# Optimization experiments

Hardware: AMD Instinct MI355X
Metric: run time of the kernel (lower is better)

The kernel has to match this reference:

```python
import jax, jax.numpy as jnp
import numpy as np

B, H, V, L, T = 64, 512, 32000, 3, 38
SOS = 0  # word2idx['<SOS>']


def setup_inputs() -> dict:
    key = jax.random.key(0)
    ks = jax.random.split(key, 16)
    s = 0.05
    rn = lambda k, shape: jax.random.normal(k, shape, jnp.float32) * s
    return {
        "feat": jax.random.normal(ks[0], (B, H), jnp.float32),
        "W_ih0": rn(ks[1], (4 * H, 2 * H)),
        "W_hh0": rn(ks[2], (4 * H, H)),
        "W_ih_rest": rn(ks[3], (L - 1, 4 * H, H)),
        "W_hh_rest": rn(ks[4], (L - 1, 4 * H, H)),
        "b_ih": rn(ks[5], (L, 4 * H)),
        "b_hh": rn(ks[6], (L, 4 * H)),
        "embed": rn(ks[7], (V, H)),
        "W_proj": rn(ks[8], (V, H)),
        "b_proj": rn(ks[9], (V,)),
        "W_hid": rn(ks[10], (H, H)),
        "b_hid": rn(ks[11], (H,)),
        "W_enc": rn(ks[12], (H, H)),
        "b_enc": rn(ks[13], (H,)),
        "W_attout": rn(ks[14], (1, H)),
        "b_attout": rn(ks[15], (1,)),
    }


def _lstm_cell(x, h, c, Wih, Whh, bih, bhh):
    # PyTorch gate order: i, f, g, o
    g = x @ Wih.T + h @ Whh.T + bih + bhh
    i, f, gg, o = jnp.split(g, 4, axis=-1)
    c2 = jax.nn.sigmoid(f) * c + jax.nn.sigmoid(i) * jnp.tanh(gg)
    h2 = jax.nn.sigmoid(o) * jnp.tanh(c2)
    return h2, c2


def _forward(feat, W_ih0, W_hh0, W_ih_rest, W_hh_rest, b_ih, b_hh,
             embed, W_proj, b_proj, W_hid, b_hid, W_enc, b_enc,
             W_attout, b_attout):
    # encoder 'sequence': pooled feature repeated over L decoder layers -> [L,B,H]
    enc = jnp.broadcast_to(feat[None], (L, B, H))
    enc_p = enc @ W_enc.T + b_enc  # precompute encoder projection (constant over steps)

    def attn(hbar):  # hbar = sum(hidden_layers)/L, [B,H]  (Bahdanau additive attention)
        e = (jnp.tanh(enc_p + (hbar @ W_hid.T + b_hid)[None]) @ W_attout.T + b_attout)[..., 0]  # [L,B]
        w = jax.nn.softmax(e, axis=0)  # softmax over encoder positions
        return jnp.einsum('lb,lbh->bh', w, enc)  # context [B,H]

    def lstm(inp, h, c):  # one time-step through the 3-layer stacked LSTM
        h0, c0 = _lstm_cell(inp, h[0], c[0], W_ih0, W_hh0, b_ih[0], b_hh[0])
        h1, c1 = _lstm_cell(h0, h[1], c[1], W_ih_rest[0], W_hh_rest[0], b_ih[1], b_hh[1])
        h2, c2 = _lstm_cell(h1, h[2], c[2], W_ih_rest[1], W_hh_rest[1], b_ih[2], b_hh[2])
        return jnp.stack([h0, h1, h2]), jnp.stack([c0, c1, c2])

    ctx0 = attn(feat)  # initial hidden = feat repeated L times -> mean = feat
    start = jnp.broadcast_to(embed[SOS], (B, H))
    h = jnp.broadcast_to(ctx0[None], (L, B, H))
    c = h
    inp0 = jnp.concatenate([ctx0, start], axis=-1)  # [B, 2H]

    def step(carry, _):
        h, c, inp = carry
        h, c = lstm(inp, h, c)
        out = h[-1]  # [B,H]
        ids = jnp.argmax(out @ W_proj.T + b_proj, axis=-1)  # greedy token (dropout in eval mode)
        emb = embed[ids]  # [B,H]
        ctx = attn(emb / L)  # addMask averages with 1/decoder_layer weights
        return (h, c, jnp.concatenate([ctx, emb], axis=-1)), out

    _, outs = jax.lax.scan(step, (h, c, inp0), None, length=T - 1)  # outs [T-1,B,H]
    pred = jnp.concatenate([start[None], outs], axis=0)  # [T,B,H]
    # final projection, permuted to [B, V, T] as in the torch module
    return jnp.einsum('tbh,vh->bvt', pred, W_proj) + b_proj[None, :, None]


def reference(feat, W_ih0, W_hh0, W_ih_rest, W_hh_rest, b_ih, b_hh,
              embed, W_proj, b_proj, W_hid, b_hid, W_enc, b_enc,
              W_attout, b_attout):
    return _forward(feat, W_ih0, W_hh0, W_ih_rest, W_hh_rest, b_ih, b_hh,
                    embed, W_proj, b_proj, W_hid, b_hid, W_enc, b_enc,
                    W_attout, b_attout)
```

## Files before the change

kernel.cpp:

```cpp
#include <hip/hip_runtime.h>
#include <hip/hip_bf16.h>

#define B   64
#define H   512
#define V   32000
#define T   38
#define G4  2048
#define NSTEP 37
#define VT  64
#define KC  64
#define LDP 68
#define NTILE 500
#define DELTA 0.008f
#define MAXC 128

typedef __attribute__((ext_vector_type(8))) short short8;
typedef __attribute__((ext_vector_type(4))) float f32x4;
typedef unsigned long long ull;

__device__ __forceinline__ float sigf(float x){ return 1.0f/(1.0f + expf(-x)); }

__device__ __forceinline__ unsigned int fkey(float x){
  unsigned int u = __float_as_uint(x);
  return (u & 0x80000000u) ? ~u : (u | 0x80000000u);
}
__device__ __forceinline__ float fromkey(unsigned int k){
  unsigned int u = (k & 0x80000000u) ? (k & 0x7fffffffu) : ~k;
  return __uint_as_float(u);
}
__device__ __forceinline__ ull mkkey(float v, int idx){
  return ((ull)fkey(v)<<32) | (ull)(unsigned int)(~(unsigned int)idx);
}
__device__ __forceinline__ unsigned short f2bf(float x){
  unsigned int u = __float_as_uint(x);
  unsigned int r = (u + 0x7FFFu + ((u >> 16) & 1u)) >> 16;
  return (unsigned short)r;
}
__device__ __forceinline__ float bf2f(unsigned short u){
  return __uint_as_float((unsigned int)u << 16);
}

__global__ __launch_bounds__(256) void k_init_state(const float* __restrict__ feat,
                                                    float* __restrict__ hT, float* __restrict__ cT,
                                                    ull* __restrict__ packed){
  int idx = blockIdx.x*blockDim.x + threadIdx.x;
  if (idx < 3*H*B){
    int b = idx & (B-1);
    int k = (idx >> 6) & (H-1);
    float v = feat[(size_t)b*H + k];
    hT[idx] = v;
    cT[idx] = v;
  }
  if (idx < NSTEP*B) packed[idx] = 0ULL;
}

__global__ __launch_bounds__(256) void k_convW(const float* __restrict__ src,
                                               unsigned short* __restrict__ hi,
                                               unsigned short* __restrict__ lo){
  int i = blockIdx.x*blockDim.x + threadIdx.x;
  float4 f = ((const float4*)src)[i];
  ushort4 h4, l4;
  h4.x = f2bf(f.x); l4.x = f2bf(f.x - bf2f(h4.x));
  h4.y = f2bf(f.y); l4.y = f2bf(f.y - bf2f(h4.y));
  h4.z = f2bf(f.z); l4.z = f2bf(f.z - bf2f(h4.z));
  h4.w = f2bf(f.w); l4.w = f2bf(f.w - bf2f(h4.w));
  ((ushort4*)hi)[i] = h4;
  ((ushort4*)lo)[i] = l4;
}

__global__ __launch_bounds__(256) void k_gfeat(const float* __restrict__ feat,
                                               const float* __restrict__ Wih0,
                                               const float* __restrict__ b_ih,
                                               const float* __restrict__ b_hh,
                                               float* __restrict__ gfeatT){
  int j = blockIdx.x;
  int b = threadIdx.x;
  int gate = threadIdx.y;
  int r = gate*H + j;
  const float* w = Wih0 + (size_t)r*(2*H);
  const float* x = feat + (size_t)b*H;
  float acc = 0.f;
  #pragma unroll 4
  for (int k=0;k<H;k++) acc = fmaf(w[k], x[k], acc);
  gfeatT[((size_t)gate*H + j)*B + b] = acc + b_ih[r] + b_hh[r];
}

__global__ __launch_bounds__(256) void k_row0(const float* __restrict__ embed_,
                                              const float* __restrict__ Wp,
                                              const float* __restrict__ bp,
                                              unsigned short* __restrict__ dstBf,
                                              float* __restrict__ dstF, int mode){
  int v = blockIdx.x*blockDim.x + threadIdx.x;
  if (v >= V) return;
  const float4* e = (const float4*)embed_;
  const float4* w = (const float4*)(Wp + (size_t)v*H);
  float acc = 0.f;
  #pragma unroll 4
  for (int k=0;k<H/4;k++){
    float4 a = e[k], c = w[k];
    acc += a.x*c.x + a.y*c.y + a.z*c.z + a.w*c.w;
  }
  acc += bp[v];
  if (mode == 0){
    unsigned short bv = f2bf(acc);
    for (int b=0;b<B;b++) dstBf[(size_t)b*V + v] = bv;
  } else {
    for (int b=0;b<B;b++) dstF[((size_t)b*V + v)*T] = acc;
  }
}

__global__ __launch_bounds__(256) void k_lstm(int layer, int s,
    const float* __restrict__ Wih, const float* __restrict__ Whh,
    const float* __restrict__ bias_ih, const float* __restrict__ bias_hh,
    const float* __restrict__ gfeatT,
    const float* __restrict__ embed_,
    const ull* __restrict__ packedPrev,
    const float* __restrict__ xLowerT,
    const float* __restrict__ hOldT,
    float* __restrict__ hNewT,
    float* __restrict__ cT_,
    unsigned short* __restrict__ hBf,
    float* __restrict__ hF)
{
  const int j  = blockIdx.x;
  const int b  = threadIdx.x;
  const int ks = threadIdx.y;
  __shared__ float part[4][4][B];

  const int kbase = (ks & 1)*256;
  const float *w0,*w1,*w2,*w3;
  const float* xptr = nullptr;
  const float* eptr = nullptr;

  if (ks < 2){
    if (layer == 0){
      const size_t gs = (size_t)H*(2*H);
      w0 = Wih + (size_t)j*(2*H) + H + kbase;
      w1 = w0 + gs; w2 = w0 + 2*gs; w3 = w0 + 3*gs;
      int er = 0;
      if (s > 0) er = (int)(~(unsigned int)(packedPrev[b] & 0xFFFFFFFFull));
      eptr = embed_ + (size_t)er*H + kbase;
    } else {
      const size_t gs = (size_t)H*H;
      w0 = Wih + (size_t)j*H + kbase;
      w1 = w0 + gs; w2 = w0 + 2*gs; w3 = w0 + 3*gs;
      xptr = xLowerT + (size_t)kbase*B + b;
    }
  } else {
    const size_t gs = (size_t)H*H;
    w0 = Whh + (size_t)j*H + kbase;
    w1 = w0 + gs; w2 = w0 + 2*gs; w3 = w0 + 3*gs;
    xptr = hOldT + (size_t)kbase*B + b;
  }

  float a0=0.f, a1=0.f, a2=0.f, a3=0.f;
  if (eptr){
    #pragma unroll 4
    for (int k=0;k<256;k++){
      float xv = eptr[k];
      a0 = fmaf(w0[k], xv, a0); a1 = fmaf(w1[k], xv, a1);
      a2 = fmaf(w2[k], xv, a2); a3 = fmaf(w3[k], xv, a3);
    }
  } else {
    #pragma unroll 4
    for (int k=0;k<256;k++){
      float xv = xptr[(size_t)k*B];
      a0 = fmaf(w0[k], xv, a0); a1 = fmaf(w1[k], xv, a1);
      a2 = fmaf(w2[k], xv, a2); a3 = fmaf(w3[k], xv, a3);
    }
  }
  part[ks][0][b]=a0; part[ks][1][b]=a1; part[ks][2][b]=a2; part[ks][3][b]=a3;
  __syncthreads();

  if (ks == 0){
    float g[4];
    #pragma unroll
    for (int gt=0; gt<4; gt++){
      float sum = part[0][gt][b] + part[1][gt][b] + part[2][gt][b] + part[3][gt][b];
      if (layer == 0) sum += gfeatT[((size_t)gt*H + j)*B + b];
      else            sum += bias_ih[gt*H + j] + bias_hh[gt*H + j];
      g[gt] = sum;
    }
    float i_ = sigf(g[0]);
    float f_ = sigf(g[1]);
    float gg = tanhf(g[2]);
    float o_ = sigf(g[3]);
    float cold = cT_[(size_t)j*B + b];
    float c2 = f_*cold + i_*gg;
    float h2 = o_*tanhf(c2);
    cT_[(size_t)j*B + b]  = c2;
    hNewT[(size_t)j*B + b] = h2;
    if (hBf){
      unsigned short hi = f2bf(h2);
      hBf[(size_t)b*H + j] = hi;
      hBf[(size_t)B*H + (size_t)b*H + j] = f2bf(h2 - bf2f(hi));
    }
    if (hF) hF[(size_t)b*H + j] = h2;
  }
}

__global__ __launch_bounds__(256, 2) void k_logits_mfma(
    const unsigned short* __restrict__ Whi,
    const unsigned short* __restrict__ Wlo,
    const unsigned short* __restrict__ h2,
    const float* __restrict__ bp,
    unsigned short* __restrict__ dst,
    ull* __restrict__ tilemax)
{
  const int tid  = threadIdx.x;
  const int wave = tid >> 6;
  const int lane = tid & 63;
  const int col  = lane & 15;
  const int grp  = lane >> 4;
  const int v0   = blockIdx.x*64 + wave*16;

  f32x4 acc[4] = {{0.f,0.f,0.f,0.f},{0.f,0.f,0.f,0.f},
                  {0.f,0.f,0.f,0.f},{0.f,0.f,0.f,0.f}};

  const unsigned short* hp  = h2 + (size_t)col*H + grp*8;
  const unsigned short* hpl = hp + (size_t)B*H;
  const unsigned short* wph = Whi + (size_t)(v0+col)*H + grp*8;
  const unsigned short* wpl = Wlo + (size_t)(v0+col)*H + grp*8;

  for (int k0 = 0; k0 < H; k0 += 32){
    short8 ah[4], al[4], bh, bl;
    #pragma unroll
    for (int bt=0;bt<4;bt++){
      ah[bt] = *(const short8*)(hp  + (size_t)bt*16*H + k0);
      al[bt] = *(const short8*)(hpl + (size_t)bt*16*H + k0);
    }
    bh = *(const short8*)(wph + k0);
    bl = *(const short8*)(wpl + k0);
    #pragma unroll
    for (int bt=0;bt<4;bt++){
      acc[bt] = __builtin_amdgcn_mfma_f32_16x16x32_bf16(ah[bt], bh, acc[bt], 0,0,0);
      acc[bt] = __builtin_amdgcn_mfma_f32_16x16x32_bf16(al[bt], bh, acc[bt], 0,0,0);
      acc[bt] = __builtin_amdgcn_mfma_f32_16x16x32_bf16(ah[bt], bl, acc[bt], 0,0,0);
    }
  }

  const float bias = bp[v0 + col];
  ull keys[4][4];
  #pragma unroll
  for (int bt=0;bt<4;bt++){
    #pragma unroll
    for (int r=0;r<4;r++){
      int b = bt*16 + grp*4 + r;
      float val = acc[bt][r] + bias;
      dst[(size_t)b*V + v0 + col] = f2bf(val);
      keys[bt][r] = mkkey(val, v0+col);
    }
  }
  #pragma unroll
  for (int bt=0;bt<4;bt++)
    #pragma unroll
    for (int r=0;r<4;r++){
      ull k2 = keys[bt][r];
      #pragma unroll
      for (int m=1;m<16;m<<=1){
        ull o = __shfl_xor(k2, m, 64);
        if (o > k2) k2 = o;
      }
      keys[bt][r] = k2;
    }

  __shared__ ull wred[4][64];
  if (col == 0){
    #pragma unroll
    for (int bt=0;bt<4;bt++)
      #pragma unroll
      for (int r=0;r<4;r++)
        wred[wave][bt*16 + grp*4 + r] = keys[bt][r];
  }
  __syncthreads();
  if (tid < 64){
    ull best = wred[0][tid];
    #pragma unroll
    for (int w=1;w<4;w++) if (wred[w][tid] > best) best = wred[w][tid];
    tilemax[(size_t)blockIdx.x*B + tid] = best;
  }
}

__global__ __launch_bounds__(256) void k_rescue(
    const unsigned short* __restrict__ plane,
    const ull* __restrict__ tilemax,
    const float* __restrict__ hF,
    const float* __restrict__ Wp,
    const float* __restrict__ bp,
    ull* __restrict__ packedS)
{
  const int b    = blockIdx.x;
  const int tid  = threadIdx.x;
  const int lane = tid & 63;
  const int wave = tid >> 6;

  __shared__ float hrow[H];
  __shared__ ull   keybuf[256];
  __shared__ int   tlist[NTILE];
  __shared__ int   vlist[MAXC];
  __shared__ ull   ckey[MAXC];
  __shared__ int   tcount, vcount;

  for (int k=tid; k<H; k+=256) hrow[k] = hF[(size_t)b*H + k];
  ull myk0 = (tid < NTILE) ? tilemax[(size_t)tid*B + b] : 0ULL;
  ull myk1 = (tid+256 < NTILE) ? tilemax[(size_t)(tid+256)*B + b] : 0ULL;
  keybuf[tid] = (myk0 > myk1) ? myk0 : myk1;
  if (tid == 0){ tcount = 0; vcount = 0; }
  __syncthreads();
  #pragma unroll
  for (int s=128; s>0; s>>=1){
    if (tid < s){ ull o = keybuf[tid+s]; if (o > keybuf[tid]) keybuf[tid] = o; }
    __syncthreads();
  }
  const float gmax   = fromkey((unsigned int)(keybuf[0] >> 32));
  const float thresh = gmax - DELTA;

  if (fromkey((unsigned int)(myk0 >> 32)) >= thresh && tid < NTILE){
    int i = atomicAdd(&tcount, 1); tlist[i] = tid;
  }
  if (fromkey((unsigned int)(myk1 >> 32)) >= thresh && tid+256 < NTILE){
    int i = atomicAdd(&tcount, 1); tlist[i] = tid+256;
  }
  __syncthreads();

  const int nt = tcount;
  for (int ti=0; ti<nt; ti++){
    if (tid < 64){
      int v = tlist[ti]*64 + tid;
      float val = bf2f(plane[(size_t)b*V + v]);
      if (val >= thresh){
        int i = atomicAdd(&vcount, 1);
        if (i < MAXC) vlist[i] = v;
      }
    }
  }
  __syncthreads();
  const int nc = min(vcount, MAXC);

  for (int base=0; base<nc; base+=4){
    int i = base + wave;
    if (i < nc){
      int v = vlist[i];
      const float* wrow = Wp + (size_t)v*H;
      float acc = 0.f;
      #pragma unroll
      for (int k=lane; k<H; k+=64) acc = fmaf(wrow[k], hrow[k], acc);
      #pragma unroll
      for (int m=32; m>0; m>>=1) acc += __shfl_xor(acc, m, 64);
      if (lane == 0) ckey[i] = mkkey(acc + bp[v], v);
    }
  }
  __syncthreads();
  if (tid == 0){
    ull best = 0ULL;
    for (int i=0;i<nc;i++) if (ckey[i] > best) best = ckey[i];
    packedS[b] = best;
  }
}

__global__ __launch_bounds__(256) void k_logits(
    const float* __restrict__ h2T,
    const float* __restrict__ Wp,
    const float* __restrict__ bp,
    float* __restrict__ dst, int strideV, int strideB,
    ull* __restrict__ packedS)
{
  __shared__ float Wt[KC][LDP];
  __shared__ float Xt[KC][LDP];
  __shared__ ull red[B][17];

  const int tid = threadIdx.x;
  const int v0  = blockIdx.x * VT;
  const int tv  = tid & 15;
  const int tb  = tid >> 4;
  const int vr  = tid >> 2;
  const int kq  = tid & 3;

  float acc[4][4];
  #pragma unroll
  for (int i=0;i<4;i++)
    #pragma unroll
    for (int q=0;q<4;q++) acc[i][q] = 0.f;

  for (int k0=0; k0<H; k0+=KC){
    __syncthreads();
    const float* wsrc = Wp + (size_t)(v0+vr)*H + k0 + kq*16;
    #pragma unroll
    for (int i=0;i<4;i++){
      float4 w4 = *(const float4*)(wsrc + i*4);
      int kk = kq*16 + i*4;
      Wt[kk+0][vr]=w4.x; Wt[kk+1][vr]=w4.y; Wt[kk+2][vr]=w4.z; Wt[kk+3][vr]=w4.w;
    }
    const float* xsrc = h2T + (size_t)(k0+vr)*B + kq*16;
    #pragma unroll
    for (int i=0;i<4;i++){
      float4 x4 = *(const float4*)(xsrc + i*4);
      int bb = kq*16 + i*4;
      Xt[vr][bb+0]=x4.x; Xt[vr][bb+1]=x4.y; Xt[vr][bb+2]=x4.z; Xt[vr][bb+3]=x4.w;
    }
    __syncthreads();
    #pragma unroll 8
    for (int k=0;k<KC;k++){
      float4 w4 = *(const float4*)&Wt[k][tv<<2];
      float4 x4 = *(const float4*)&Xt[k][tb<<2];
      acc[0][0]=fmaf(x4.x,w4.x,acc[0][0]); acc[0][1]=fmaf(x4.x,w4.y,acc[0][1]);
      acc[0][2]=fmaf(x4.x,w4.z,acc[0][2]); acc[0][3]=fmaf(x4.x,w4.w,acc[0][3]);
      acc[1][0]=fmaf(x4.y,w4.x,acc[1][0]); acc[1][1]=fmaf(x4.y,w4.y,acc[1][1]);
      acc[1][2]=fmaf(x4.y,w4.z,acc[1][2]); acc[1][3]=fmaf(x4.y,w4.w,acc[1][3]);
      acc[2][0]=fmaf(x4.z,w4.x,acc[2][0]); acc[2][1]=fmaf(x4.z,w4.y,acc[2][1]);
      acc[2][2]=fmaf(x4.z,w4.z,acc[2][2]); acc[2][3]=fmaf(x4.z,w4.w,acc[2][3]);
      acc[3][0]=fmaf(x4.w,w4.x,acc[3][0]); acc[3][1]=fmaf(x4.w,w4.y,acc[3][1]);
      acc[3][2]=fmaf(x4.w,w4.z,acc[3][2]); acc[3][3]=fmaf(x4.w,w4.w,acc[3][3]);
    }
  }

  float4 bb4 = *(const float4*)(bp + v0 + (tv<<2));
  float barr[4] = {bb4.x, bb4.y, bb4.z, bb4.w};
  float vals[4][4];
  #pragma unroll
  for (int bj=0;bj<4;bj++)
    #pragma unroll
    for (int vi=0;vi<4;vi++) vals[bj][vi] = acc[bj][vi] + barr[vi];

  #pragma unroll
  for (int bj=0;bj<4;bj++){
    int b = (tb<<2)+bj;
    #pragma unroll
    for (int vi=0;vi<4;vi++)
      dst[(size_t)b*strideB + (size_t)(v0+(tv<<2)+vi)*strideV] = vals[bj][vi];
  }

  #pragma unroll
  for (int bj=0;bj<4;bj++){
    float m = vals[bj][0]; int mi = v0+(tv<<2);
    #pragma unroll
    for (int vi=1;vi<4;vi++){
      if (vals[bj][vi] > m){ m = vals[bj][vi]; mi = v0+(tv<<2)+vi; }
    }
    red[(tb<<2)+bj][tv] = mkkey(m, mi);
  }
  __syncthreads();
  if (tid < B){
    ull best = red[tid][0];
    #pragma unroll
    for (int t2=1;t2<16;t2++){ ull k2 = red[tid][t2]; if (k2 > best) best = k2; }
    atomicMax(packedS + tid, best);
  }
}

__global__ __launch_bounds__(256) void k_transpose(const unsigned short* __restrict__ stage,
                                                   float* __restrict__ out){
  __shared__ float tile[64][40];
  const int b  = blockIdx.x / (V/64);
  const int vt = blockIdx.x % (V/64);
  const int v0 = vt*64;
  const int tid = threadIdx.x;

  for (int idx = tid; idx < T*64; idx += 256){
    int t  = idx >> 6;
    int vl = idx & 63;
    tile[vl][t] = bf2f(stage[(size_t)t*B*V + (size_t)b*V + v0 + vl]);
  }
  __syncthreads();

  float* obase = out + ((size_t)b*V + v0)*T;
  for (int idx = tid; idx < (T*64)/4; idx += 256){
    int e = idx*4;
    float4 o;
    o.x = tile[(e+0)/T][(e+0)%T];
    o.y = tile[(e+1)/T][(e+1)%T];
    o.z = tile[(e+2)/T][(e+2)%T];
    o.w = tile[(e+3)/T][(e+3)%T];
    *(float4*)(obase + e) = o;
  }
}

extern "C" void kernel_launch(void* const* d_in, const int* in_sizes, int n_in,
                              void* d_out, int out_size, void* d_ws, size_t ws_size,
                              hipStream_t stream){
  const float* feat      = (const float*)d_in[0];
  const float* W_ih0     = (const float*)d_in[1];
  const float* W_hh0     = (const float*)d_in[2];
  const float* W_ih_rest = (const float*)d_in[3];
  const float* W_hh_rest = (const float*)d_in[4];
  const float* b_ih      = (const float*)d_in[5];
  const float* b_hh      = (const float*)d_in[6];
  const float* embed     = (const float*)d_in[7];
  const float* W_proj    = (const float*)d_in[8];
  const float* b_proj    = (const float*)d_in[9];
  float* out = (float*)d_out;

  char* ws = (char*)d_ws;
  size_t off = 0;
  float* hT = (float*)(ws + off); off += (size_t)2*3*H*B*4;
  float* cT = (float*)(ws + off); off += (size_t)3*H*B*4;
  float* gfeatT = (float*)(ws + off); off += (size_t)4*H*B*4;
  ull* packed = (ull*)(ws + off); off += (size_t)NSTEP*B*8;
  unsigned short* h2bf = (unsigned short*)(ws + off); off += (size_t)2*B*H*2;
  float* hF32 = (float*)(ws + off); off += (size_t)B*H*4;
  ull* tilemax = (ull*)(ws + off); off += (size_t)NTILE*B*8;
  off = (off + 255) & ~(size_t)255;
  unsigned short* Whi = (unsigned short*)(ws + off); off += (size_t)V*H*2;
  unsigned short* Wlo = (unsigned short*)(ws + off); off += (size_t)V*H*2;
  off = (off + 255) & ~(size_t)255;
  unsigned short* stage = (unsigned short*)(ws + off);
  const size_t need = off + (size_t)T*B*V*2;
  const bool fast = (ws_size >= need);

  dim3 bl64x4(64,4);
  k_init_state<<<(3*H*B + 255)/256, 256, 0, stream>>>(feat, hT, cT, packed);
  k_gfeat<<<H, bl64x4, 0, stream>>>(feat, W_ih0, b_ih, b_hh, gfeatT);
  if (fast){
    k_convW<<<(V*H/4)/256, 256, 0, stream>>>(W_proj, Whi, Wlo);
    k_row0<<<(V+255)/256, 256, 0, stream>>>(embed, W_proj, b_proj, stage, (float*)nullptr, 0);
  } else {
    k_row0<<<(V+255)/256, 256, 0, stream>>>(embed, W_proj, b_proj, (unsigned short*)nullptr, out, 1);
  }

  const size_t LHB = (size_t)H*B;
  for (int s=0; s<NSTEP; s++){
    const int p = s & 1, q = p ^ 1;
    float* hOld = hT + (size_t)p*3*LHB;
    float* hNew = hT + (size_t)q*3*LHB;
    const ull* pk = packed + (size_t)(s>0 ? s-1 : 0)*B;

    k_lstm<<<H, bl64x4, 0, stream>>>(0, s, W_ih0, W_hh0,
        b_ih, b_hh, gfeatT, embed, pk,
        (const float*)nullptr, hOld + 0*LHB, hNew + 0*LHB, cT + 0*LHB,
        (unsigned short*)nullptr, (float*)nullptr);
    k_lstm<<<H, bl64x4, 0, stream>>>(1, s, W_ih_rest, W_hh_rest,
        b_ih + 1*G4, b_hh + 1*G4, (const float*)nullptr, (const float*)nullptr,
        (const ull*)nullptr,
        hNew + 0*LHB, hOld + 1*LHB, hNew + 1*LHB, cT + 1*LHB,
        (unsigned short*)nullptr, (float*)nullptr);
    k_lstm<<<H, bl64x4, 0, stream>>>(2, s, W_ih_rest + (size_t)G4*H, W_hh_rest + (size_t)G4*H,
        b_ih + 2*G4, b_hh + 2*G4, (const float*)nullptr, (const float*)nullptr,
        (const ull*)nullptr,
        hNew + 1*LHB, hOld + 2*LHB, hNew + 2*LHB, cT + 2*LHB,
        fast ? h2bf : (unsigned short*)nullptr,
        fast ? hF32 : (float*)nullptr);

    if (fast){
      unsigned short* plane = stage + (size_t)(s+1)*B*V;
      k_logits_mfma<<<NTILE, 256, 0, stream>>>(Whi, Wlo, h2bf, b_proj, plane, tilemax);
      k_rescue<<<B, 256, 0, stream>>>(plane, tilemax, hF32, W_proj, b_proj,
                                      packed + (size_t)s*B);
    } else {
      k_logits<<<V/VT, 256, 0, stream>>>(hNew + 2*LHB, W_proj, b_proj,
          out + (s+1), T, V*T, packed + (size_t)s*B);
    }
  }

  if (fast) k_transpose<<<B*(V/64), 256, 0, stream>>>(stage, out);
}
```

Baseline: 4.819 ms.

## Fuse per-step LSTM, logits and argmax rescue into one kernel with grid barriers

Each decode step used to launch five kernels (three LSTM layers, the MFMA logits pass and the argmax rescue). They are merged into a single 512-block kernel per step, with a software grid barrier (atomic counter plus generation) between the phases. This removes four launches and their inter-kernel gaps per step. In exchange it depends on all 512 blocks being co-resident, otherwise the barrier deadlocks. It also adds barrier spin and fence costs.

```diff
diff --git a/kernel.cpp b/kernel.cpp
--- a/kernel.cpp
+++ b/kernel.cpp
@@ -13,6 +13,7 @@
 #define NTILE 500
 #define DELTA 0.008f
 #define MAXC 128
+#define GRID 512
 
 typedef __attribute__((ext_vector_type(8))) short short8;
 typedef __attribute__((ext_vector_type(4))) float f32x4;
@@ -40,9 +41,27 @@
   return __uint_as_float((unsigned int)u << 16);
 }
 
+__device__ __forceinline__ void gridbar(unsigned int* bar){
+  __syncthreads();
+  if (threadIdx.x == 0){
+    __threadfence();
+    unsigned int gen = __hip_atomic_load(bar+1, __ATOMIC_RELAXED, __HIP_MEMORY_SCOPE_AGENT);
+    if (__hip_atomic_fetch_add(bar, 1u, __ATOMIC_ACQ_REL, __HIP_MEMORY_SCOPE_AGENT) == GRID-1u){
+      __hip_atomic_store(bar, 0u, __ATOMIC_RELAXED, __HIP_MEMORY_SCOPE_AGENT);
+      __hip_atomic_fetch_add(bar+1, 1u, __ATOMIC_RELEASE, __HIP_MEMORY_SCOPE_AGENT);
+    } else {
+      while (__hip_atomic_load(bar+1, __ATOMIC_RELAXED, __HIP_MEMORY_SCOPE_AGENT) == gen)
+        __builtin_amdgcn_s_sleep(8);
+    }
+    __threadfence();
+  }
+  __syncthreads();
+}
+
 __global__ __launch_bounds__(256) void k_init_state(const float* __restrict__ feat,
                                                     float* __restrict__ hT, float* __restrict__ cT,
-                                                    ull* __restrict__ packed){
+                                                    ull* __restrict__ packed,
+                                                    unsigned int* __restrict__ bar){
   int idx = blockIdx.x*blockDim.x + threadIdx.x;
   if (idx < 3*H*B){
     int b = idx & (B-1);
@@ -52,6 +71,7 @@
     cT[idx] = v;
   }
   if (idx < NSTEP*B) packed[idx] = 0ULL;
+  if (idx < 2) bar[idx] = 0u;
 }
 
 __global__ __launch_bounds__(256) void k_convW(const float* __restrict__ src,
@@ -109,6 +129,258 @@
   }
 }
 
+__global__ __launch_bounds__(256, 2) void k_step(
+    int s,
+    const float* __restrict__ W_ih0, const float* __restrict__ W_hh0,
+    const float* __restrict__ W_ih_rest, const float* __restrict__ W_hh_rest,
+    const float* __restrict__ b_ih, const float* __restrict__ b_hh,
+    const float* __restrict__ gfeatT,
+    const float* __restrict__ embed_,
+    const ull* __restrict__ pk,
+    const float* __restrict__ hOld,
+    float* __restrict__ hNew,
+    float* __restrict__ cT_,
+    unsigned short* __restrict__ h2bf,
+    float* __restrict__ hF32,
+    const unsigned short* __restrict__ Whi,
+    const unsigned short* __restrict__ Wlo,
+    const float* __restrict__ bp,
+    unsigned short* __restrict__ plane,
+    ull* __restrict__ tilemax,
+    const float* __restrict__ WpF,
+    ull* __restrict__ packedS,
+    unsigned int* __restrict__ bar)
+{
+  const int blk = blockIdx.x;
+  const int tid = threadIdx.x;
+
+  __shared__ float part[4][4][B];
+  __shared__ ull   wred[4][64];
+  __shared__ float hrow[H];
+  __shared__ ull   keybuf[256];
+  __shared__ int   tlist[NTILE];
+  __shared__ int   vlist[MAXC];
+  __shared__ ull   ckey[MAXC];
+  __shared__ int   tcount, vcount;
+
+  {
+    const int b  = tid & 63;
+    const int ks = tid >> 6;
+    const int j  = blk;
+    for (int layer = 0; layer < 3; ++layer){
+      const int kbase = (ks & 1)*256;
+      const float* w0;
+      const float* xptr = nullptr;
+      const float* eptr = nullptr;
+      size_t gs;
+      if (ks < 2){
+        if (layer == 0){
+          gs = (size_t)H*(2*H);
+          w0 = W_ih0 + (size_t)j*(2*H) + H + kbase;
+          int er = 0;
+          if (s > 0) er = (int)(~(unsigned int)(pk[b] & 0xFFFFFFFFull));
+          eptr = embed_ + (size_t)er*H + kbase;
+        } else {
+          gs = (size_t)H*H;
+          const float* Wihl = (layer==1) ? W_ih_rest : (W_ih_rest + (size_t)G4*H);
+          w0 = Wihl + (size_t)j*H + kbase;
+          xptr = hNew + (size_t)(layer-1)*H*B + (size_t)kbase*B + b;
+        }
+      } else {
+        gs = (size_t)H*H;
+        const float* Whhl = (layer==0) ? W_hh0 :
+                            ((layer==1) ? W_hh_rest : (W_hh_rest + (size_t)G4*H));
+        w0 = Whhl + (size_t)j*H + kbase;
+        xptr = hOld + (size_t)layer*H*B + (size_t)kbase*B + b;
+      }
+      const float* w1 = w0 + gs;
+      const float* w2 = w0 + 2*gs;
+      const float* w3 = w0 + 3*gs;
+
+      float a0=0.f, a1=0.f, a2=0.f, a3=0.f;
+      if (eptr){
+        #pragma unroll 4
+        for (int k=0;k<256;k++){
+          float xv = eptr[k];
+          a0 = fmaf(w0[k], xv, a0); a1 = fmaf(w1[k], xv, a1);
+          a2 = fmaf(w2[k], xv, a2); a3 = fmaf(w3[k], xv, a3);
+        }
+      } else {
+        #pragma unroll 4
+        for (int k=0;k<256;k++){
+          float xv = xptr[(size_t)k*B];
+          a0 = fmaf(w0[k], xv, a0); a1 = fmaf(w1[k], xv, a1);
+          a2 = fmaf(w2[k], xv, a2); a3 = fmaf(w3[k], xv, a3);
+        }
+      }
+      part[ks][0][b]=a0; part[ks][1][b]=a1; part[ks][2][b]=a2; part[ks][3][b]=a3;
+      __syncthreads();
+
+      if (ks == 0){
+        float g[4];
+        #pragma unroll
+        for (int gt=0; gt<4; gt++){
+          float sum = part[0][gt][b] + part[1][gt][b] + part[2][gt][b] + part[3][gt][b];
+          if (layer == 0) sum += gfeatT[((size_t)gt*H + j)*B + b];
+          else            sum += b_ih[layer*G4 + gt*H + j] + b_hh[layer*G4 + gt*H + j];
+          g[gt] = sum;
+        }
+        float i_ = sigf(g[0]);
+        float f_ = sigf(g[1]);
+        float gg = tanhf(g[2]);
+        float o_ = sigf(g[3]);
+        float cold = cT_[(size_t)layer*H*B + (size_t)j*B + b];
+        float c2 = f_*cold + i_*gg;
+        float h2 = o_*tanhf(c2);
+        cT_[(size_t)layer*H*B + (size_t)j*B + b]  = c2;
+        hNew[(size_t)layer*H*B + (size_t)j*B + b] = h2;
+        if (layer == 2){
+          unsigned short hi = f2bf(h2);
+          h2bf[(size_t)b*H + j] = hi;
+          h2bf[(size_t)B*H + (size_t)b*H + j] = f2bf(h2 - bf2f(hi));
+          hF32[(size_t)b*H + j] = h2;
+        }
+      }
+      gridbar(bar);
+    }
+  }
+
+  if (blk < NTILE){
+    const int wave = tid >> 6;
+    const int lane = tid & 63;
+    const int col  = lane & 15;
+    const int grp  = lane >> 4;
+    const int v0   = blk*64 + wave*16;
+
+    f32x4 acc[4] = {{0.f,0.f,0.f,0.f},{0.f,0.f,0.f,0.f},
+                    {0.f,0.f,0.f,0.f},{0.f,0.f,0.f,0.f}};
+
+    const unsigned short* hp  = h2bf + (size_t)col*H + grp*8;
+    const unsigned short* hpl = hp + (size_t)B*H;
+    const unsigned short* wph = Whi + (size_t)(v0+col)*H + grp*8;
+    const unsigned short* wpl = Wlo + (size_t)(v0+col)*H + grp*8;
+
+    for (int k0 = 0; k0 < H; k0 += 32){
+      short8 ah[4], al[4], bh, bl;
+      #pragma unroll
+      for (int bt=0;bt<4;bt++){
+        ah[bt] = *(const short8*)(hp  + (size_t)bt*16*H + k0);
+        al[bt] = *(const short8*)(hpl + (size_t)bt*16*H + k0);
+      }
+      bh = *(const short8*)(wph + k0);
+      bl = *(const short8*)(wpl + k0);
+      #pragma unroll
+      for (int bt=0;bt<4;bt++){
+        acc[bt] = __builtin_amdgcn_mfma_f32_16x16x32_bf16(ah[bt], bh, acc[bt], 0,0,0);
+        acc[bt] = __builtin_amdgcn_mfma_f32_16x16x32_bf16(al[bt], bh, acc[bt], 0,0,0);
+        acc[bt] = __builtin_amdgcn_mfma_f32_16x16x32_bf16(ah[bt], bl, acc[bt], 0,0,0);
+      }
+    }
+
+    const float bias = bp[v0 + col];
+    ull keys[4][4];
+    #pragma unroll
+    for (int bt=0;bt<4;bt++){
+      #pragma unroll
+      for (int r=0;r<4;r++){
+        int b = bt*16 + grp*4 + r;
+        float val = acc[bt][r] + bias;
+        plane[(size_t)b*V + v0 + col] = f2bf(val);
+        keys[bt][r] = mkkey(val, v0+col);
+      }
+    }
+    #pragma unroll
+    for (int bt=0;bt<4;bt++)
+      #pragma unroll
+      for (int r=0;r<4;r++){
+        ull k2 = keys[bt][r];
+        #pragma unroll
+        for (int m=1;m<16;m<<=1){
+          ull o = __shfl_xor(k2, m, 64);
+          if (o > k2) k2 = o;
+        }
+        keys[bt][r] = k2;
+      }
+    if (col == 0){
+      #pragma unroll
+      for (int bt=0;bt<4;bt++)
+        #pragma unroll
+        for (int r=0;r<4;r++)
+          wred[wave][bt*16 + grp*4 + r] = keys[bt][r];
+    }
+    __syncthreads();
+    if (tid < 64){
+      ull best = wred[0][tid];
+      #pragma unroll
+      for (int w=1;w<4;w++) if (wred[w][tid] > best) best = wred[w][tid];
+      tilemax[(size_t)blk*B + tid] = best;
+    }
+  }
+  gridbar(bar);
+
+  if (blk < B){
+    const int b    = blk;
+    const int lane = tid & 63;
+    const int wave = tid >> 6;
+
+    for (int k=tid; k<H; k+=256) hrow[k] = hF32[(size_t)b*H + k];
+    ull myk0 = (tid < NTILE) ? tilemax[(size_t)tid*B + b] : 0ULL;
+    ull myk1 = (tid+256 < NTILE) ? tilemax[(size_t)(tid+256)*B + b] : 0ULL;
+    keybuf[tid] = (myk0 > myk1) ? myk0 : myk1;
+    if (tid == 0){ tcount = 0; vcount = 0; }
+    __syncthreads();
+    #pragma unroll
+    for (int st=128; st>0; st>>=1){
+      if (tid < st){ ull o = keybuf[tid+st]; if (o > keybuf[tid]) keybuf[tid] = o; }
+      __syncthreads();
+    }
+    const float gmax   = fromkey((unsigned int)(keybuf[0] >> 32));
+    const float thresh = gmax - DELTA;
+
+    if (fromkey((unsigned int)(myk0 >> 32)) >= thresh && tid < NTILE){
+      int i = atomicAdd(&tcount, 1); tlist[i] = tid;
+    }
+    if (fromkey((unsigned int)(myk1 >> 32)) >= thresh && tid+256 < NTILE){
+      int i = atomicAdd(&tcount, 1); tlist[i] = tid+256;
+    }
+    __syncthreads();
+
+    const int nt = tcount;
+    for (int ti=0; ti<nt; ti++){
+      if (tid < 64){
+        int v = tlist[ti]*64 + tid;
+        float val = bf2f(plane[(size_t)b*V + v]);
+        if (val >= thresh){
+          int i = atomicAdd(&vcount, 1);
+          if (i < MAXC) vlist[i] = v;
+        }
+      }
+    }
+    __syncthreads();
+    const int nc = min(vcount, MAXC);
+
+    for (int base=0; base<nc; base+=4){
+      int i = base + wave;
+      if (i < nc){
+        int v = vlist[i];
+        const float* wrow = WpF + (size_t)v*H;
+        float acc = 0.f;
+        #pragma unroll
+        for (int k=lane; k<H; k+=64) acc = fmaf(wrow[k], hrow[k], acc);
+        #pragma unroll
+        for (int m=32; m>0; m>>=1) acc += __shfl_xor(acc, m, 64);
+        if (lane == 0) ckey[i] = mkkey(acc + bp[v], v);
+      }
+    }
+    __syncthreads();
+    if (tid == 0){
+      ull best = 0ULL;
+      for (int i=0;i<nc;i++) if (ckey[i] > best) best = ckey[i];
+      packedS[b] = best;
+    }
+  }
+}
+
 __global__ __launch_bounds__(256) void k_lstm(int layer, int s,
     const float* __restrict__ Wih, const float* __restrict__ Whh,
     const float* __restrict__ bias_ih, const float* __restrict__ bias_hh,
@@ -118,9 +390,7 @@
     const float* __restrict__ xLowerT,
     const float* __restrict__ hOldT,
     float* __restrict__ hNewT,
-    float* __restrict__ cT_,
-    unsigned short* __restrict__ hBf,
-    float* __restrict__ hF)
+    float* __restrict__ cT_)
 {
   const int j  = blockIdx.x;
   const int b  = threadIdx.x;
@@ -190,171 +460,6 @@
     float h2 = o_*tanhf(c2);
     cT_[(size_t)j*B + b]  = c2;
     hNewT[(size_t)j*B + b] = h2;
-    if (hBf){
-      unsigned short hi = f2bf(h2);
-      hBf[(size_t)b*H + j] = hi;
-      hBf[(size_t)B*H + (size_t)b*H + j] = f2bf(h2 - bf2f(hi));
-    }
-    if (hF) hF[(size_t)b*H + j] = h2;
-  }
-}
-
-__global__ __launch_bounds__(256, 2) void k_logits_mfma(
-    const unsigned short* __restrict__ Whi,
-    const unsigned short* __restrict__ Wlo,
-    const unsigned short* __restrict__ h2,
-    const float* __restrict__ bp,
-    unsigned short* __restrict__ dst,
-    ull* __restrict__ tilemax)
-{
-  const int tid  = threadIdx.x;
-  const int wave = tid >> 6;
-  const int lane = tid & 63;
-  const int col  = lane & 15;
-  const int grp  = lane >> 4;
-  const int v0   = blockIdx.x*64 + wave*16;
-
-  f32x4 acc[4] = {{0.f,0.f,0.f,0.f},{0.f,0.f,0.f,0.f},
-                  {0.f,0.f,0.f,0.f},{0.f,0.f,0.f,0.f}};
-
-  const unsigned short* hp  = h2 + (size_t)col*H + grp*8;
-  const unsigned short* hpl = hp + (size_t)B*H;
-  const unsigned short* wph = Whi + (size_t)(v0+col)*H + grp*8;
-  const unsigned short* wpl = Wlo + (size_t)(v0+col)*H + grp*8;
-
-  for (int k0 = 0; k0 < H; k0 += 32){
-    short8 ah[4], al[4], bh, bl;
-    #pragma unroll
-    for (int bt=0;bt<4;bt++){
-      ah[bt] = *(const short8*)(hp  + (size_t)bt*16*H + k0);
-      al[bt] = *(const short8*)(hpl + (size_t)bt*16*H + k0);
-    }
-    bh = *(const short8*)(wph + k0);
-    bl = *(const short8*)(wpl + k0);
-    #pragma unroll
-    for (int bt=0;bt<4;bt++){
-      acc[bt] = __builtin_amdgcn_mfma_f32_16x16x32_bf16(ah[bt], bh, acc[bt], 0,0,0);
-      acc[bt] = __builtin_amdgcn_mfma_f32_16x16x32_bf16(al[bt], bh, acc[bt], 0,0,0);
-      acc[bt] = __builtin_amdgcn_mfma_f32_16x16x32_bf16(ah[bt], bl, acc[bt], 0,0,0);
-    }
-  }
-
-  const float bias = bp[v0 + col];
-  ull keys[4][4];
-  #pragma unroll
-  for (int bt=0;bt<4;bt++){
-    #pragma unroll
-    for (int r=0;r<4;r++){
-      int b = bt*16 + grp*4 + r;
-      float val = acc[bt][r] + bias;
-      dst[(size_t)b*V + v0 + col] = f2bf(val);
-      keys[bt][r] = mkkey(val, v0+col);
-    }
-  }
-  #pragma unroll
-  for (int bt=0;bt<4;bt++)
-    #pragma unroll
-    for (int r=0;r<4;r++){
-      ull k2 = keys[bt][r];
-      #pragma unroll
-      for (int m=1;m<16;m<<=1){
-        ull o = __shfl_xor(k2, m, 64);
-        if (o > k2) k2 = o;
-      }
-      keys[bt][r] = k2;
-    }
-
-  __shared__ ull wred[4][64];
-  if (col == 0){
-    #pragma unroll
-    for (int bt=0;bt<4;bt++)
-      #pragma unroll
-      for (int r=0;r<4;r++)
-        wred[wave][bt*16 + grp*4 + r] = keys[bt][r];
-  }
-  __syncthreads();
-  if (tid < 64){
-    ull best = wred[0][tid];
-    #pragma unroll
-    for (int w=1;w<4;w++) if (wred[w][tid] > best) best = wred[w][tid];
-    tilemax[(size_t)blockIdx.x*B + tid] = best;
-  }
-}
-
-__global__ __launch_bounds__(256) void k_rescue(
-    const unsigned short* __restrict__ plane,
-    const ull* __restrict__ tilemax,
-    const float* __restrict__ hF,
-    const float* __restrict__ Wp,
-    const float* __restrict__ bp,
-    ull* __restrict__ packedS)
-{
-  const int b    = blockIdx.x;
-  const int tid  = threadIdx.x;
-  const int lane = tid & 63;
-  const int wave = tid >> 6;
-
-  __shared__ float hrow[H];
-  __shared__ ull   keybuf[256];
-  __shared__ int   tlist[NTILE];
-  __shared__ int   vlist[MAXC];
-  __shared__ ull   ckey[MAXC];
-  __shared__ int   tcount, vcount;
-
-  for (int k=tid; k<H; k+=256) hrow[k] = hF[(size_t)b*H + k];
-  ull myk0 = (tid < NTILE) ? tilemax[(size_t)tid*B + b] : 0ULL;
-  ull myk1 = (tid+256 < NTILE) ? tilemax[(size_t)(tid+256)*B + b] : 0ULL;
-  keybuf[tid] = (myk0 > myk1) ? myk0 : myk1;
-  if (tid == 0){ tcount = 0; vcount = 0; }
-  __syncthreads();
-  #pragma unroll
-  for (int s=128; s>0; s>>=1){
-    if (tid < s){ ull o = keybuf[tid+s]; if (o > keybuf[tid]) keybuf[tid] = o; }
-    __syncthreads();
-  }
-  const float gmax   = fromkey((unsigned int)(keybuf[0] >> 32));
-  const float thresh = gmax - DELTA;
-
-  if (fromkey((unsigned int)(myk0 >> 32)) >= thresh && tid < NTILE){
-    int i = atomicAdd(&tcount, 1); tlist[i] = tid;
-  }
-  if (fromkey((unsigned int)(myk1 >> 32)) >= thresh && tid+256 < NTILE){
-    int i = atomicAdd(&tcount, 1); tlist[i] = tid+256;
-  }
-  __syncthreads();
-
-  const int nt = tcount;
-  for (int ti=0; ti<nt; ti++){
-    if (tid < 64){
-      int v = tlist[ti]*64 + tid;
-      float val = bf2f(plane[(size_t)b*V + v]);
-      if (val >= thresh){
-        int i = atomicAdd(&vcount, 1);
-        if (i < MAXC) vlist[i] = v;
-      }
-    }
-  }
-  __syncthreads();
-  const int nc = min(vcount, MAXC);
-
-  for (int base=0; base<nc; base+=4){
-    int i = base + wave;
-    if (i < nc){
-      int v = vlist[i];
-      const float* wrow = Wp + (size_t)v*H;
-      float acc = 0.f;
-      #pragma unroll
-      for (int k=lane; k<H; k+=64) acc = fmaf(wrow[k], hrow[k], acc);
-      #pragma unroll
-      for (int m=32; m>0; m>>=1) acc += __shfl_xor(acc, m, 64);
-      if (lane == 0) ckey[i] = mkkey(acc + bp[v], v);
-    }
-  }
-  __syncthreads();
-  if (tid == 0){
-    ull best = 0ULL;
-    for (int i=0;i<nc;i++) if (ckey[i] > best) best = ckey[i];
-    packedS[b] = best;
   }
 }
 
@@ -499,6 +604,7 @@
   unsigned short* h2bf = (unsigned short*)(ws + off); off += (size_t)2*B*H*2;
   float* hF32 = (float*)(ws + off); off += (size_t)B*H*4;
   ull* tilemax = (ull*)(ws + off); off += (size_t)NTILE*B*8;
+  unsigned int* bar = (unsigned int*)(ws + off); off += 256;
   off = (off + 255) & ~(size_t)255;
   unsigned short* Whi = (unsigned short*)(ws + off); off += (size_t)V*H*2;
   unsigned short* Wlo = (unsigned short*)(ws + off); off += (size_t)V*H*2;
@@ -508,48 +614,47 @@
   const bool fast = (ws_size >= need);
 
   dim3 bl64x4(64,4);
-  k_init_state<<<(3*H*B + 255)/256, 256, 0, stream>>>(feat, hT, cT, packed);
+  k_init_state<<<(3*H*B + 255)/256, 256, 0, stream>>>(feat, hT, cT, packed, bar);
   k_gfeat<<<H, bl64x4, 0, stream>>>(feat, W_ih0, b_ih, b_hh, gfeatT);
+
+  const size_t LHB = (size_t)H*B;
   if (fast){
     k_convW<<<(V*H/4)/256, 256, 0, stream>>>(W_proj, Whi, Wlo);
     k_row0<<<(V+255)/256, 256, 0, stream>>>(embed, W_proj, b_proj, stage, (float*)nullptr, 0);
+
+    for (int s=0; s<NSTEP; s++){
+      const int p = s & 1, q = p ^ 1;
+      k_step<<<GRID, 256, 0, stream>>>(s,
+          W_ih0, W_hh0, W_ih_rest, W_hh_rest, b_ih, b_hh,
+          gfeatT, embed, packed + (size_t)(s>0 ? s-1 : 0)*B,
+          hT + (size_t)p*3*LHB, hT + (size_t)q*3*LHB, cT,
+          h2bf, hF32, Whi, Wlo, b_proj,
+          stage + (size_t)(s+1)*B*V, tilemax,
+          W_proj, packed + (size_t)s*B, bar);
+    }
+    k_transpose<<<B*(V/64), 256, 0, stream>>>(stage, out);
   } else {
     k_row0<<<(V+255)/256, 256, 0, stream>>>(embed, W_proj, b_proj, (unsigned short*)nullptr, out, 1);
-  }
-
-  const size_t LHB = (size_t)H*B;
-  for (int s=0; s<NSTEP; s++){
-    const int p = s & 1, q = p ^ 1;
-    float* hOld = hT + (size_t)p*3*LHB;
-    float* hNew = hT + (size_t)q*3*LHB;
-    const ull* pk = packed + (size_t)(s>0 ? s-1 : 0)*B;
-
-    k_lstm<<<H, bl64x4, 0, stream>>>(0, s, W_ih0, W_hh0,
-        b_ih, b_hh, gfeatT, embed, pk,
-        (const float*)nullptr, hOld + 0*LHB, hNew + 0*LHB, cT + 0*LHB,
-        (unsigned short*)nullptr, (float*)nullptr);
-    k_lstm<<<H, bl64x4, 0, stream>>>(1, s, W_ih_rest, W_hh_rest,
-        b_ih + 1*G4, b_hh + 1*G4, (const float*)nullptr, (const float*)nullptr,
-        (const ull*)nullptr,
-        hNew + 0*LHB, hOld + 1*LHB, hNew + 1*LHB, cT + 1*LHB,
-        (unsigned short*)nullptr, (float*)nullptr);
-    k_lstm<<<H, bl64x4, 0, stream>>>(2, s, W_ih_rest + (size_t)G4*H, W_hh_rest + (size_t)G4*H,
-        b_ih + 2*G4, b_hh + 2*G4, (const float*)nullptr, (const float*)nullptr,
-        (const ull*)nullptr,
-        hNew + 1*LHB, hOld + 2*LHB, hNew + 2*LHB, cT + 2*LHB,
-        fast ? h2bf : (unsigned short*)nullptr,
-        fast ? hF32 : (float*)nullptr);
-
-    if (fast){
-      unsigned short* plane = stage + (size_t)(s+1)*B*V;
-      k_logits_mfma<<<NTILE, 256, 0, stream>>>(Whi, Wlo, h2bf, b_proj, plane, tilemax);
-      k_rescue<<<B, 256, 0, stream>>>(plane, tilemax, hF32, W_proj, b_proj,
-                                      packed + (size_t)s*B);
-    } else {
+    for (int s=0; s<NSTEP; s++){
+      const int p = s & 1, q = p ^ 1;
+      float* hOld = hT + (size_t)p*3*LHB;
+      float* hNew = hT + (size_t)q*3*LHB;
+      const ull* pk = packed + (size_t)(s>0 ? s-1 : 0)*B;
+
+      k_lstm<<<H, bl64x4, 0, stream>>>(0, s, W_ih0, W_hh0,
+          b_ih, b_hh, gfeatT, embed, pk,
+          (const float*)nullptr, hOld + 0*LHB, hNew + 0*LHB, cT + 0*LHB);
+      k_lstm<<<H, bl64x4, 0, stream>>>(1, s, W_ih_rest, W_hh_rest,
+          b_ih + 1*G4, b_hh + 1*G4, (const float*)nullptr, (const float*)nullptr,
+          (const ull*)nullptr,
+          hNew + 0*LHB, hOld + 1*LHB, hNew + 1*LHB, cT + 1*LHB);
+      k_lstm<<<H, bl64x4, 0, stream>>>(2, s, W_ih_rest + (size_t)G4*H, W_hh_rest + (size_t)G4*H,
+          b_ih + 2*G4, b_hh + 2*G4, (const float*)nullptr, (const float*)nullptr,
+          (const ull*)nullptr,
+          hNew + 1*LHB, hOld + 2*LHB, hNew + 2*LHB, cT + 2*LHB);
+
       k_logits<<<V/VT, 256, 0, stream>>>(hNew + 2*LHB, W_proj, b_proj,
           out + (s+1), T, V*T, packed + (size_t)s*B);
     }
   }
-
-  if (fast) k_transpose<<<B*(V/64), 256, 0, stream>>>(stage, out);
-}
+}
```

After: 11.51 ms. 139% more time.

## Drop split-bf16 logits GEMM, widen tiles, use nontemporal stores

Applied to the files above, without the earlier changes.

Replaces the three-MFMA hi/lo split-bf16 logits computation with a single plain bf16 MFMA. It also doubles the vocabulary tile per block to 128 columns, which halves the tile count, and transposes the tilemax layout so the rescue kernel reads it contiguously. Staging writes and transpose reads/writes now use nontemporal stores and loads. Precision of the logits drops, and the existing fp32 rescue pass with its DELTA threshold is relied on to still recover the exact argmax.

```diff
diff --git a/kernel.cpp b/kernel.cpp
--- a/kernel.cpp
+++ b/kernel.cpp
@@ -10,7 +10,7 @@
 #define VT  64
 #define KC  64
 #define LDP 68
-#define NTILE 500
+#define NTILE 250
 #define DELTA 0.008f
 #define MAXC 128
 
@@ -55,17 +55,11 @@
 }
 
 __global__ __launch_bounds__(256) void k_convW(const float* __restrict__ src,
-                                               unsigned short* __restrict__ hi,
-                                               unsigned short* __restrict__ lo){
+                                               unsigned short* __restrict__ hi){
   int i = blockIdx.x*blockDim.x + threadIdx.x;
   float4 f = ((const float4*)src)[i];
-  ushort4 h4, l4;
-  h4.x = f2bf(f.x); l4.x = f2bf(f.x - bf2f(h4.x));
-  h4.y = f2bf(f.y); l4.y = f2bf(f.y - bf2f(h4.y));
-  h4.z = f2bf(f.z); l4.z = f2bf(f.z - bf2f(h4.z));
-  h4.w = f2bf(f.w); l4.w = f2bf(f.w - bf2f(h4.w));
+  ushort4 h4 = make_ushort4(f2bf(f.x), f2bf(f.y), f2bf(f.z), f2bf(f.w));
   ((ushort4*)hi)[i] = h4;
-  ((ushort4*)lo)[i] = l4;
 }
 
 __global__ __launch_bounds__(256) void k_gfeat(const float* __restrict__ feat,
@@ -103,7 +97,7 @@
   acc += bp[v];
   if (mode == 0){
     unsigned short bv = f2bf(acc);
-    for (int b=0;b<B;b++) dstBf[(size_t)b*V + v] = bv;
+    for (int b=0;b<B;b++) __builtin_nontemporal_store(bv, dstBf + (size_t)b*V + v);
   } else {
     for (int b=0;b<B;b++) dstF[((size_t)b*V + v)*T] = acc;
   }
@@ -190,19 +184,14 @@
     float h2 = o_*tanhf(c2);
     cT_[(size_t)j*B + b]  = c2;
     hNewT[(size_t)j*B + b] = h2;
-    if (hBf){
-      unsigned short hi = f2bf(h2);
-      hBf[(size_t)b*H + j] = hi;
-      hBf[(size_t)B*H + (size_t)b*H + j] = f2bf(h2 - bf2f(hi));
-    }
-    if (hF) hF[(size_t)b*H + j] = h2;
-  }
-}
-
-__global__ __launch_bounds__(256, 2) void k_logits_mfma(
-    const unsigned short* __restrict__ Whi,
-    const unsigned short* __restrict__ Wlo,
-    const unsigned short* __restrict__ h2,
+    if (hBf) hBf[(size_t)b*H + j] = f2bf(h2);
+    if (hF)  hF [(size_t)b*H + j] = h2;
+  }
+}
+
+__global__ __launch_bounds__(256) void k_logits_mfma(
+    const unsigned short* __restrict__ Wbf,
+    const unsigned short* __restrict__ h2bf,
     const float* __restrict__ bp,
     unsigned short* __restrict__ dst,
     ull* __restrict__ tilemax)
@@ -212,43 +201,47 @@
   const int lane = tid & 63;
   const int col  = lane & 15;
   const int grp  = lane >> 4;
-  const int v0   = blockIdx.x*64 + wave*16;
-
-  f32x4 acc[4] = {{0.f,0.f,0.f,0.f},{0.f,0.f,0.f,0.f},
-                  {0.f,0.f,0.f,0.f},{0.f,0.f,0.f,0.f}};
-
-  const unsigned short* hp  = h2 + (size_t)col*H + grp*8;
-  const unsigned short* hpl = hp + (size_t)B*H;
-  const unsigned short* wph = Whi + (size_t)(v0+col)*H + grp*8;
-  const unsigned short* wpl = Wlo + (size_t)(v0+col)*H + grp*8;
+  const int v0   = blockIdx.x*128 + wave*32;
+
+  f32x4 acc[4][2] = {{{0.f,0.f,0.f,0.f},{0.f,0.f,0.f,0.f}},
+                     {{0.f,0.f,0.f,0.f},{0.f,0.f,0.f,0.f}},
+                     {{0.f,0.f,0.f,0.f},{0.f,0.f,0.f,0.f}},
+                     {{0.f,0.f,0.f,0.f},{0.f,0.f,0.f,0.f}}};
+
+  const unsigned short* hp = h2bf + (size_t)col*H + grp*8;
+  const unsigned short* wp = Wbf  + (size_t)(v0+col)*H + grp*8;
 
   for (int k0 = 0; k0 < H; k0 += 32){
-    short8 ah[4], al[4], bh, bl;
-    #pragma unroll
-    for (int bt=0;bt<4;bt++){
-      ah[bt] = *(const short8*)(hp  + (size_t)bt*16*H + k0);
-      al[bt] = *(const short8*)(hpl + (size_t)bt*16*H + k0);
-    }
-    bh = *(const short8*)(wph + k0);
-    bl = *(const short8*)(wpl + k0);
-    #pragma unroll
-    for (int bt=0;bt<4;bt++){
-      acc[bt] = __builtin_amdgcn_mfma_f32_16x16x32_bf16(ah[bt], bh, acc[bt], 0,0,0);
-      acc[bt] = __builtin_amdgcn_mfma_f32_16x16x32_bf16(al[bt], bh, acc[bt], 0,0,0);
-      acc[bt] = __builtin_amdgcn_mfma_f32_16x16x32_bf16(ah[bt], bl, acc[bt], 0,0,0);
-    }
-  }
-
-  const float bias = bp[v0 + col];
+    short8 afr[4], bfr[2];
+    #pragma unroll
+    for (int bt=0;bt<4;bt++)
+      afr[bt] = *(const short8*)(hp + (size_t)bt*16*H + k0);
+    #pragma unroll
+    for (int vt=0;vt<2;vt++)
+      bfr[vt] = *(const short8*)(wp + (size_t)vt*16*H + k0);
+    #pragma unroll
+    for (int bt=0;bt<4;bt++)
+      #pragma unroll
+      for (int vt=0;vt<2;vt++)
+        acc[bt][vt] = __builtin_amdgcn_mfma_f32_16x16x32_bf16(afr[bt], bfr[vt], acc[bt][vt], 0,0,0);
+  }
+
+  float bias0 = bp[v0 + col];
+  float bias1 = bp[v0 + 16 + col];
+
   ull keys[4][4];
   #pragma unroll
   for (int bt=0;bt<4;bt++){
     #pragma unroll
     for (int r=0;r<4;r++){
       int b = bt*16 + grp*4 + r;
-      float val = acc[bt][r] + bias;
-      dst[(size_t)b*V + v0 + col] = f2bf(val);
-      keys[bt][r] = mkkey(val, v0+col);
+      float val0 = acc[bt][0][r] + bias0;
+      float val1 = acc[bt][1][r] + bias1;
+      __builtin_nontemporal_store(f2bf(val0), dst + (size_t)b*V + v0 + col);
+      __builtin_nontemporal_store(f2bf(val1), dst + (size_t)b*V + v0 + 16 + col);
+      float m; int mv;
+      if (val1 > val0){ m = val1; mv = v0+16+col; } else { m = val0; mv = v0+col; }
+      keys[bt][r] = mkkey(m, mv);
     }
   }
   #pragma unroll
@@ -277,7 +270,7 @@
     ull best = wred[0][tid];
     #pragma unroll
     for (int w=1;w<4;w++) if (wred[w][tid] > best) best = wred[w][tid];
-    tilemax[(size_t)blockIdx.x*B + tid] = best;
+    tilemax[(size_t)tid*NTILE + blockIdx.x] = best;
   }
 }
 
@@ -302,31 +295,27 @@
   __shared__ int   tcount, vcount;
 
   for (int k=tid; k<H; k+=256) hrow[k] = hF[(size_t)b*H + k];
-  ull myk0 = (tid < NTILE) ? tilemax[(size_t)tid*B + b] : 0ULL;
-  ull myk1 = (tid+256 < NTILE) ? tilemax[(size_t)(tid+256)*B + b] : 0ULL;
-  keybuf[tid] = (myk0 > myk1) ? myk0 : myk1;
+  ull myk = (tid < NTILE) ? tilemax[(size_t)b*NTILE + tid] : 0ULL;
+  keybuf[tid] = myk;
   if (tid == 0){ tcount = 0; vcount = 0; }
   __syncthreads();
   #pragma unroll
-  for (int s=128; s>0; s>>=1){
-    if (tid < s){ ull o = keybuf[tid+s]; if (o > keybuf[tid]) keybuf[tid] = o; }
+  for (int st=128; st>0; st>>=1){
+    if (tid < st){ ull o = keybuf[tid+st]; if (o > keybuf[tid]) keybuf[tid] = o; }
     __syncthreads();
   }
   const float gmax   = fromkey((unsigned int)(keybuf[0] >> 32));
   const float thresh = gmax - DELTA;
 
-  if (fromkey((unsigned int)(myk0 >> 32)) >= thresh && tid < NTILE){
+  if (tid < NTILE && fromkey((unsigned int)(myk >> 32)) >= thresh){
     int i = atomicAdd(&tcount, 1); tlist[i] = tid;
-  }
-  if (fromkey((unsigned int)(myk1 >> 32)) >= thresh && tid+256 < NTILE){
-    int i = atomicAdd(&tcount, 1); tlist[i] = tid+256;
   }
   __syncthreads();
 
   const int nt = tcount;
   for (int ti=0; ti<nt; ti++){
-    if (tid < 64){
-      int v = tlist[ti]*64 + tid;
+    if (tid < 128){
+      int v = tlist[ti]*128 + tid;
       float val = bf2f(plane[(size_t)b*V + v]);
       if (val >= thresh){
         int i = atomicAdd(&vcount, 1);
@@ -459,19 +448,20 @@
   for (int idx = tid; idx < T*64; idx += 256){
     int t  = idx >> 6;
     int vl = idx & 63;
-    tile[vl][t] = bf2f(stage[(size_t)t*B*V + (size_t)b*V + v0 + vl]);
+    unsigned short u = __builtin_nontemporal_load(stage + (size_t)t*B*V + (size_t)b*V + v0 + vl);
+    tile[vl][t] = bf2f(u);
   }
   __syncthreads();
 
   float* obase = out + ((size_t)b*V + v0)*T;
   for (int idx = tid; idx < (T*64)/4; idx += 256){
     int e = idx*4;
-    float4 o;
-    o.x = tile[(e+0)/T][(e+0)%T];
-    o.y = tile[(e+1)/T][(e+1)%T];
-    o.z = tile[(e+2)/T][(e+2)%T];
-    o.w = tile[(e+3)/T][(e+3)%T];
-    *(float4*)(obase + e) = o;
+    f32x4 o;
+    o[0] = tile[(e+0)/T][(e+0)%T];
+    o[1] = tile[(e+1)/T][(e+1)%T];
+    o[2] = tile[(e+2)/T][(e+2)%T];
+    o[3] = tile[(e+3)/T][(e+3)%T];
+    __builtin_nontemporal_store(o, (f32x4*)(obase + e));
   }
 }
 
@@ -496,12 +486,11 @@
   float* cT = (float*)(ws + off); off += (size_t)3*H*B*4;
   float* gfeatT = (float*)(ws + off); off += (size_t)4*H*B*4;
   ull* packed = (ull*)(ws + off); off += (size_t)NSTEP*B*8;
-  unsigned short* h2bf = (unsigned short*)(ws + off); off += (size_t)2*B*H*2;
+  unsigned short* h2bf = (unsigned short*)(ws + off); off += (size_t)B*H*2;
   float* hF32 = (float*)(ws + off); off += (size_t)B*H*4;
-  ull* tilemax = (ull*)(ws + off); off += (size_t)NTILE*B*8;
+  ull* tilemax = (ull*)(ws + off); off += (size_t)B*NTILE*8;
   off = (off + 255) & ~(size_t)255;
   unsigned short* Whi = (unsigned short*)(ws + off); off += (size_t)V*H*2;
-  unsigned short* Wlo = (unsigned short*)(ws + off); off += (size_t)V*H*2;
   off = (off + 255) & ~(size_t)255;
   unsigned short* stage = (unsigned short*)(ws + off);
   const size_t need = off + (size_t)T*B*V*2;
@@ -511,7 +500,7 @@
   k_init_state<<<(3*H*B + 255)/256, 256, 0, stream>>>(feat, hT, cT, packed);
   k_gfeat<<<H, bl64x4, 0, stream>>>(feat, W_ih0, b_ih, b_hh, gfeatT);
   if (fast){
-    k_convW<<<(V*H/4)/256, 256, 0, stream>>>(W_proj, Whi, Wlo);
+    k_convW<<<(V*H/4)/256, 256, 0, stream>>>(W_proj, Whi);
     k_row0<<<(V+255)/256, 256, 0, stream>>>(embed, W_proj, b_proj, stage, (float*)nullptr, 0);
   } else {
     k_row0<<<(V+255)/256, 256, 0, stream>>>(embed, W_proj, b_proj, (unsigned short*)nullptr, out, 1);
@@ -542,7 +531,7 @@
 
     if (fast){
       unsigned short* plane = stage + (size_t)(s+1)*B*V;
-      k_logits_mfma<<<NTILE, 256, 0, stream>>>(Whi, Wlo, h2bf, b_proj, plane, tilemax);
+      k_logits_mfma<<<NTILE, 256, 0, stream>>>(Whi, h2bf, b_proj, plane, tilemax);
       k_rescue<<<B, 256, 0, stream>>>(plane, tilemax, hF32, W_proj, b_proj,
                                       packed + (size_t)s*B);
     } else {
```

Measured after the change: 3.893 ms, median of 2. -19.2%, faster.
